# Kernel optimization log

Measured on AMD Instinct MI355X. Metric: run time of the kernel, lower is better.

The kernel has to match this reference:

```python
import jax, jax.numpy as jnp
import numpy as np

N = 50000
IN_DIM = 512
NEG_SLOPE = 0.2


def gat_conv(x, src, dst, W, a_src, a_dst, bias, heads, out_c, concat):
    # x: [N, F_in]; src/dst: [E] (self-loops already appended)
    n = x.shape[0]
    h = (x @ W).reshape(n, heads, out_c)              # [N,H,C]
    alpha_s = (h * a_src).sum(-1)                     # [N,H]
    alpha_d = (h * a_dst).sum(-1)                     # [N,H]
    e = jax.nn.leaky_relu(alpha_s[src] + alpha_d[dst], NEG_SLOPE)  # [E,H]
    # segment softmax over destination node neighborhoods
    m = jax.ops.segment_max(e, dst, num_segments=n)
    e = jnp.exp(e - m[dst])
    denom = jax.ops.segment_sum(e, dst, num_segments=n)
    alpha = e / (denom[dst] + 1e-16)                  # [E,H]
    msg = h[src] * alpha[:, :, None]                  # [E,H,C]
    out = jax.ops.segment_sum(msg, dst, num_segments=n)  # [N,H,C]
    out = out.reshape(n, heads * out_c) if concat else out.mean(axis=1)
    return out + bias


def setup_inputs() -> dict:
    key = jax.random.key(0)
    ks = jax.random.split(key, 16)
    E = 1600000
    txt = jax.random.normal(ks[0], (N, 768), dtype=jnp.float32)
    x = jax.random.normal(ks[1], (N, IN_DIM), dtype=jnp.float32)
    edge_index = jax.random.randint(ks[2], (2, E), 0, N, dtype=jnp.int64)
    s = lambda fan: 1.0 / np.sqrt(fan)
    W1 = jax.random.normal(ks[3], (IN_DIM, 4 * 32), dtype=jnp.float32) * s(IN_DIM)
    a_src1 = jax.random.normal(ks[4], (4, 32), dtype=jnp.float32) * s(32)
    a_dst1 = jax.random.normal(ks[5], (4, 32), dtype=jnp.float32) * s(32)
    b1 = jnp.zeros((4 * 32,), dtype=jnp.float32)
    W2 = jax.random.normal(ks[6], (128, 32), dtype=jnp.float32) * s(128)
    a_src2 = jax.random.normal(ks[7], (1, 32), dtype=jnp.float32) * s(32)
    a_dst2 = jax.random.normal(ks[8], (1, 32), dtype=jnp.float32) * s(32)
    b2 = jnp.zeros((32,), dtype=jnp.float32)
    Wf1 = jax.random.normal(ks[9], (768 + 32, 64), dtype=jnp.float32) * s(800)
    bf1 = jnp.zeros((64,), dtype=jnp.float32)
    Wf2 = jax.random.normal(ks[10], (64, 1), dtype=jnp.float32) * s(64)
    bf2 = jnp.zeros((1,), dtype=jnp.float32)
    return {"txt": txt, "x": x, "W1": W1, "a_src1": a_src1, "a_dst1": a_dst1,
            "b1": b1, "W2": W2, "a_src2": a_src2, "a_dst2": a_dst2, "b2": b2,
            "Wf1": Wf1, "bf1": bf1, "Wf2": Wf2, "bf2": bf2,
            "edge_index": edge_index}


def reference(txt, x, W1, a_src1, a_dst1, b1, W2, a_src2, a_dst2, b2,
              Wf1, bf1, Wf2, bf2, edge_index):
    # PyG GATConv adds self-loops by default
    loops = jnp.arange(N, dtype=edge_index.dtype)
    src = jnp.concatenate([edge_index[0], loops])
    dst = jnp.concatenate([edge_index[1], loops])
    h1 = gat_conv(x, src, dst, W1, a_src1, a_dst1, b1, 4, 32, True)    # [N,128]
    h1 = jax.nn.elu(h1)
    g = gat_conv(h1, src, dst, W2, a_src2, a_dst2, b2, 1, 32, False)   # [N,32]
    z = jnp.concatenate([txt, g], axis=1)                              # [N,800]
    z = jax.nn.relu(z @ Wf1 + bf1)
    out = (z @ Wf2 + bf2).squeeze(-1)                                  # [N]
    return out
```

## Files before the change

### kernel.cpp

```cpp
#include <hip/hip_runtime.h>
#include <hip/hip_bf16.h>
#include <cstdint>

#define NEG_SLOPE 0.2f
#define BCAP 16384

typedef __bf16 bf16_t;
typedef __bf16 bf16x8 __attribute__((ext_vector_type(8)));
typedef float f32x4 __attribute__((ext_vector_type(4)));
typedef float f32x2 __attribute__((ext_vector_type(2)));

__device__ __forceinline__ uint2 pack4bf16(float4 v) {
    ushort u0 = __builtin_bit_cast(ushort, (bf16_t)v.x);
    ushort u1 = __builtin_bit_cast(ushort, (bf16_t)v.y);
    ushort u2 = __builtin_bit_cast(ushort, (bf16_t)v.z);
    ushort u3 = __builtin_bit_cast(ushort, (bf16_t)v.w);
    uint2 r;
    r.x = (uint)u0 | ((uint)u1 << 16);
    r.y = (uint)u2 | ((uint)u3 << 16);
    return r;
}

__device__ __forceinline__ float bflo(uint u) { return __builtin_bit_cast(float, u << 16); }
__device__ __forceinline__ float bfhi(uint u) { return __builtin_bit_cast(float, u & 0xFFFF0000u); }


__device__ void bucket_dev(char* smem, int b, const int* __restrict__ ei, int E, int n,
                           int nbuck, unsigned* __restrict__ gcur, unsigned* __restrict__ gbuck) {
    unsigned* stage = (unsigned*)smem;
    unsigned* cnt   = stage + 4096;
    unsigned* sc    = cnt + 256;
    unsigned* offx  = sc + 256;
    unsigned* gbase = offx + 256;
    int tid = threadIdx.x;
    int ET = E + n;
    int tileStart = b * 4096;
    cnt[tid] = 0;
    __syncthreads();
    unsigned pk[16];
    int rk[16];
    #pragma unroll
    for (int i = 0; i < 16; ++i) {
        int idx = tileStart + i * 256 + tid;
        rk[i] = -1;
        if (idx < ET) {
            int s, d;
            if (idx < E) { s = ei[idx]; d = ei[E + idx]; } else { s = d = idx - E; }
            pk[i] = ((unsigned)d << 16) | (unsigned)s;
            rk[i] = (int)atomicAdd(&cnt[(unsigned)d >> 8], 1u);
        }
    }
    __syncthreads();
    sc[tid] = cnt[tid];
    __syncthreads();
    for (int off = 1; off < 256; off <<= 1) {
        unsigned t = (tid >= off) ? sc[tid - off] : 0u;
        __syncthreads();
        sc[tid] += t;
        __syncthreads();
    }
    offx[tid] = sc[tid] - cnt[tid];
    if (tid < nbuck && cnt[tid] > 0) gbase[tid] = atomicAdd(&gcur[tid], cnt[tid]);
    unsigned total = sc[255];
    __syncthreads();
    #pragma unroll
    for (int i = 0; i < 16; ++i) {
        if (rk[i] >= 0) stage[offx[pk[i] >> 24] + rk[i]] = pk[i];
    }
    __syncthreads();
    for (unsigned j = tid; j < total; j += 256) {
        unsigned p = stage[j];
        unsigned bb = p >> 24;
        unsigned pos = gbase[bb] + (j - offx[bb]);
        gbuck[(size_t)bb * BCAP + pos] = p;
    }
}

__device__ void w1t_dev(char* smem, int b, const float* __restrict__ W, bf16_t* __restrict__ Wt) {
    float (*s)[17] = (float(*)[17])smem;
    int tx = threadIdx.x & 15, ty = threadIdx.x >> 4;
    int kt = b & 31, nt = b >> 5;
    s[ty][tx] = W[(size_t)(kt * 16 + ty) * 128 + nt * 16 + tx];
    __syncthreads();
    Wt[(size_t)(nt * 16 + ty) * 512 + kt * 16 + tx] = (bf16_t)s[tx][ty];
}

__device__ void wf1t_dev(char* smem, int b, const float* __restrict__ W, bf16_t* __restrict__ Wt) {
    float (*s)[17] = (float(*)[17])smem;
    int tx = threadIdx.x & 15, ty = threadIdx.x >> 4;
    int kt = b % 52, nt = b / 52;
    int kg = kt * 16 + ty;
    s[ty][tx] = (kg < 800) ? W[(size_t)kg * 64 + nt * 16 + tx] : 0.f;
    __syncthreads();
    Wt[(size_t)(nt * 16 + ty) * 832 + kt * 16 + tx] = (bf16_t)s[tx][ty];
}

__device__ void finecsr_dev(char* smem, int b, const unsigned* __restrict__ gcur,
                            const unsigned* __restrict__ gbuck, int nbuck,
                            unsigned* __restrict__ rowptr, ushort* __restrict__ csr16) {
    unsigned* s   = (unsigned*)smem;
    unsigned* c   = s + 256;
    unsigned* sc  = c + 256;
    unsigned* cur = sc + 256;
    int tid = threadIdx.x;
    unsigned v = (tid < nbuck) ? gcur[tid] : 0u;
    s[tid] = v;
    __syncthreads();
    for (int off = 1; off < 256; off <<= 1) {
        unsigned t = (tid >= off) ? s[tid - off] : 0u;
        __syncthreads();
        s[tid] += t;
        __syncthreads();
    }
    unsigned base = s[b] - gcur[b];
    unsigned cntL = gcur[b];
    const unsigned* gb = gbuck + (size_t)b * BCAP;
    c[tid] = 0;
    __syncthreads();
    for (unsigned j = tid; j < cntL; j += 256) atomicAdd(&c[(gb[j] >> 16) & 255], 1u);
    __syncthreads();
    sc[tid] = c[tid];
    __syncthreads();
    for (int off = 1; off < 256; off <<= 1) {
        unsigned t = (tid >= off) ? sc[tid - off] : 0u;
        __syncthreads();
        sc[tid] += t;
        __syncthreads();
    }
    unsigned ox = sc[tid] - c[tid];
    rowptr[b * 256 + tid] = base + ox;
    cur[tid] = ox;
    __syncthreads();
    for (unsigned j = tid; j < cntL; j += 256) {
        unsigned p = gb[j];
        unsigned dl = (p >> 16) & 255;
        unsigned pos = atomicAdd(&cur[dl], 1u);
        csr16[base + pos] = (ushort)(p & 0xFFFFu);
    }
}

__device__ void gemm1_dev(char* smem, int b, const float* __restrict__ x,
                          const bf16_t* __restrict__ W1bt,
                          const float* __restrict__ a_src1, const float* __restrict__ a_dst1,
                          unsigned char* __restrict__ h1f8,
                          float* __restrict__ asrc, float* __restrict__ adst, int n) {
    char* As = smem;
    char* Bs = smem + 8192;
    int tid = threadIdx.x;
    int bn = b * 64;
    int wave = tid >> 6, lane = tid & 63;
    int lr = lane & 15, lk = lane >> 4;
    f32x4 acc[8] = {};
    const float4* x4 = (const float4*)x;

    for (int s = 0; s < 8; ++s) {
        int k0 = s * 64;
        #pragma unroll
        for (int i = 0; i < 4; ++i) {
            int v = tid + i * 256;
            int row = v >> 4, c4 = v & 15;
            int node = bn + row;
            float4 val = (node < n) ? x4[(size_t)node * 128 + (k0 >> 2) + c4]
                                    : make_float4(0.f, 0.f, 0.f, 0.f);
            uint off = (uint)(row * 128 + c4 * 8);
            off ^= (uint)((row & 7) << 4);
            *(uint2*)(As + off) = pack4bf16(val);
        }
        #pragma unroll
        for (int i = 0; i < 8; ++i) {
            int v = tid + i * 256;
            int row = v >> 4, c = v & 15;
            uint2 val = *(const uint2*)(W1bt + (size_t)row * 512 + k0 + c * 4);
            uint off = (uint)(row * 128 + c * 8);
            off ^= (uint)((row & 7) << 4);
            *(uint2*)(Bs + off) = val;
        }
        __syncthreads();
        #pragma unroll
        for (int ks = 0; ks < 2; ++ks) {
            uint arow = (uint)(wave * 16 + lr);
            uint aoff = (arow * 128 + (uint)(ks * 64 + lk * 16)) ^ (uint)((lr & 7) << 4);
            bf16x8 av = *(const bf16x8*)(As + aoff);
            #pragma unroll
            for (int f = 0; f < 8; ++f) {
                uint brow = (uint)(f * 16 + lr);
                uint boff = (brow * 128 + (uint)(ks * 64 + lk * 16)) ^ (uint)((lr & 7) << 4);
                bf16x8 bv = *(const bf16x8*)(Bs + boff);
                acc[f] = __builtin_amdgcn_mfma_f32_16x16x32_bf16(av, bv, acc[f], 0, 0, 0);
            }
        }
        __syncthreads();
    }
    #pragma unroll
    for (int f = 0; f < 8; ++f) {
        int nn = f * 16 + lr;
        #pragma unroll
        for (int r = 0; r < 4; ++r) {
            int node = bn + wave * 16 + lk * 4 + r;
            if (node < n) {
                float v = acc[f][r];
                uint b8 = (uint)__builtin_amdgcn_cvt_pk_fp8_f32(v, v, 0, false) & 0xFFu;
                h1f8[(size_t)node * 128 + nn] = (unsigned char)b8;
            }
        }
    }
    float asv[8], adv[8];
    #pragma unroll
    for (int h = 0; h < 4; ++h) {
        asv[2 * h]     = a_src1[h * 32 + lr];
        asv[2 * h + 1] = a_src1[h * 32 + 16 + lr];
        adv[2 * h]     = a_dst1[h * 32 + lr];
        adv[2 * h + 1] = a_dst1[h * 32 + 16 + lr];
    }
    #pragma unroll
    for (int r = 0; r < 4; ++r) {
        int node = bn + wave * 16 + lk * 4 + r;
        #pragma unroll
        for (int h = 0; h < 4; ++h) {
            float ps = acc[2 * h][r] * asv[2 * h] + acc[2 * h + 1][r] * asv[2 * h + 1];
            float pd = acc[2 * h][r] * adv[2 * h] + acc[2 * h + 1][r] * adv[2 * h + 1];
            #pragma unroll
            for (int m = 8; m >= 1; m >>= 1) {
                ps += __shfl_xor(ps, m, 64);
                pd += __shfl_xor(pd, m, 64);
            }
            if (node < n) {
                if (lr == h)     asrc[node * 4 + h] = ps;
                if (lr == h + 4) adst[node * 4 + h] = pd;
            }
        }
    }
}

__device__ void mlpA_dev(char* smem, int b, const float* __restrict__ txt,
                         const bf16_t* __restrict__ Wf1bt, float* __restrict__ hacc, int n) {
    char* As = smem;
    char* Bs = smem + 8192;
    int tid = threadIdx.x;
    int bn = b * 64;
    int wave = tid >> 6, lane = tid & 63;
    int lr = lane & 15, lk = lane >> 4;
    f32x4 acc[4] = {};
    const float4* t4 = (const float4*)txt;
    for (int s = 0; s < 12; ++s) {
        int k0 = s * 64;
        #pragma unroll
        for (int i = 0; i < 4; ++i) {
            int v = tid + i * 256;
            int row = v >> 4, c4 = v & 15;
            int node = bn + row;
            int kg = k0 + c4 * 4;
            float4 val = (node < n) ? t4[(size_t)node * 192 + (kg >> 2)]
                                    : make_float4(0.f, 0.f, 0.f, 0.f);
            uint off = (uint)(row * 128 + c4 * 8);
            off ^= (uint)((row & 7) << 4);
            *(uint2*)(As + off) = pack4bf16(val);
        }
        #pragma unroll
        for (int i = 0; i < 4; ++i) {
            int v = tid + i * 256;
            int row = v >> 4, c = v & 15;
            uint2 val = *(const uint2*)(Wf1bt + (size_t)row * 832 + k0 + c * 4);
            uint off = (uint)(row * 128 + c * 8);
            off ^= (uint)((row & 7) << 4);
            *(uint2*)(Bs + off) = val;
        }
        __syncthreads();
        #pragma unroll
        for (int ks = 0; ks < 2; ++ks) {
            uint arow = (uint)(wave * 16 + lr);
            uint aoff = (arow * 128 + (uint)(ks * 64 + lk * 16)) ^ (uint)((lr & 7) << 4);
            bf16x8 av = *(const bf16x8*)(As + aoff);
            #pragma unroll
            for (int f = 0; f < 4; ++f) {
                uint brow = (uint)(f * 16 + lr);
                uint boff = (brow * 128 + (uint)(ks * 64 + lk * 16)) ^ (uint)((lr & 7) << 4);
                bf16x8 bv = *(const bf16x8*)(Bs + boff);
                acc[f] = __builtin_amdgcn_mfma_f32_16x16x32_bf16(av, bv, acc[f], 0, 0, 0);
            }
        }
        __syncthreads();
    }
    #pragma unroll
    for (int f = 0; f < 4; ++f) {
        int nn = f * 16 + lr;
        #pragma unroll
        for (int r = 0; r < 4; ++r) {
            int node = bn + wave * 16 + lk * 4 + r;
            if (node < n) hacc[(size_t)node * 64 + nn] = acc[f][r];
        }
    }
}

__device__ void gat2_dev(char* smem, int b, const bf16_t* __restrict__ h2bf,
                         const float* __restrict__ asrc2, const float* __restrict__ adst2,
                         const float* __restrict__ b2, const unsigned* __restrict__ rowptr,
                         const ushort* __restrict__ csr16, float* __restrict__ g, int n) {
    ushort* ssm = (ushort*)smem;
    float* psm = (float*)(smem + 512);
    int tid = threadIdx.x;
    int wv = tid >> 6, l = tid & 63;
    int d = b * 4 + wv;
    if (d >= n) return;
    ushort* ss = ssm + wv * 64;
    float* ps = psm + wv * 64;
    unsigned k0 = rowptr[d], k1 = rowptr[d + 1];
    float adh = adst2[d];
    const uint2* h2u2 = (const uint2*)h2bf;
    int c = l & 7, sub = l >> 3;
    float den = 0.f, a0 = 0.f, a1 = 0.f, a2 = 0.f, a3 = 0.f;
    for (unsigned kk = k0; kk < k1; kk += 64) {
        unsigned k = kk + l;
        float p = 0.f;
        unsigned s = 0u;
        if (k < k1) {
            s = csr16[k];
            float v = asrc2[s] + adh;
            v = (v > 0.f) ? v : NEG_SLOPE * v;
            p = __expf(v);
        }
        ss[l] = (ushort)s;
        ps[l] = p;
        den += p;
        int nk = (int)min(64u, k1 - kk);
        for (int qb = 0; qb < nk; qb += 8) {
            int q = qb + sub;
            float pq = ps[q];
            uint2 u = h2u2[(unsigned)ss[q] * 8u + (unsigned)c];
            a0 = fmaf(pq, bflo(u.x), a0);
            a1 = fmaf(pq, bfhi(u.x), a1);
            a2 = fmaf(pq, bflo(u.y), a2);
            a3 = fmaf(pq, bfhi(u.y), a3);
        }
    }
    #pragma unroll
    for (int m = 32; m >= 1; m >>= 1) den += __shfl_xor(den, m, 64);
    #pragma unroll
    for (int m = 8; m <= 32; m <<= 1) {
        a0 += __shfl_xor(a0, m, 64);
        a1 += __shfl_xor(a1, m, 64);
        a2 += __shfl_xor(a2, m, 64);
        a3 += __shfl_xor(a3, m, 64);
    }
    if (l < 8) {
        float inv = 1.f / (den + 1e-16f);
        float4 bb = *(const float4*)(b2 + 4 * c);
        float4 val;
        val.x = a0 * inv + bb.x;
        val.y = a1 * inv + bb.y;
        val.z = a2 * inv + bb.z;
        val.w = a3 * inv + bb.w;
        *(float4*)(g + (size_t)d * 32 + 4 * c) = val;
    }
}


__global__ __launch_bounds__(256) void k_fuse_pre(const int* __restrict__ ei, int E, int n,
                                                  int nbuck, int ntiles,
                                                  unsigned* __restrict__ gcur,
                                                  unsigned* __restrict__ gbuck,
                                                  const float* __restrict__ W1,
                                                  bf16_t* __restrict__ W1bt,
                                                  const float* __restrict__ Wf1,
                                                  bf16_t* __restrict__ Wf1bt) {
    __shared__ __align__(16) char smem[20480];
    int b = blockIdx.x;
    if (b < ntiles)            bucket_dev(smem, b, ei, E, n, nbuck, gcur, gbuck);
    else if (b < ntiles + 256) w1t_dev(smem, b - ntiles, W1, W1bt);
    else                       wf1t_dev(smem, b - ntiles - 256, Wf1, Wf1bt);
}

__global__ __launch_bounds__(256) void k_fuse_csr_gemm(const unsigned* __restrict__ gcur,
                                                       const unsigned* __restrict__ gbuck,
                                                       int nbuck,
                                                       unsigned* __restrict__ rowptr,
                                                       ushort* __restrict__ csr16,
                                                       const float* __restrict__ x,
                                                       const bf16_t* __restrict__ W1bt,
                                                       const float* __restrict__ a_src1,
                                                       const float* __restrict__ a_dst1,
                                                       unsigned char* __restrict__ h1f8,
                                                       float* __restrict__ asrc,
                                                       float* __restrict__ adst, int n) {
    __shared__ __align__(16) char smem[24576];
    int b = blockIdx.x;
    if (b < nbuck) finecsr_dev(smem, b, gcur, gbuck, nbuck, rowptr, csr16);
    else           gemm1_dev(smem, b - nbuck, x, W1bt, a_src1, a_dst1, h1f8, asrc, adst, n);
}

__global__ __launch_bounds__(256) void k_fuse_mlpA_gat2(const float* __restrict__ txt,
                                                        const bf16_t* __restrict__ Wf1bt,
                                                        float* __restrict__ hacc, int nb64,
                                                        const bf16_t* __restrict__ h2bf,
                                                        const float* __restrict__ asrc2,
                                                        const float* __restrict__ adst2,
                                                        const float* __restrict__ b2,
                                                        const unsigned* __restrict__ rowptr,
                                                        const ushort* __restrict__ csr16,
                                                        float* __restrict__ g, int n) {
    __shared__ __align__(16) char smem[16384];
    int b = blockIdx.x;
    if (b < nb64) mlpA_dev(smem, b, txt, Wf1bt, hacc, n);
    else          gat2_dev(smem, b - nb64, h2bf, asrc2, adst2, b2, rowptr, csr16, g, n);
}

__global__ __launch_bounds__(512, 8) void k_gat1(const unsigned char* __restrict__ h1f8,
                                                 const float* __restrict__ asrc,
                                                 const float* __restrict__ adst,
                                                 const float* __restrict__ b1,
                                                 const unsigned* __restrict__ rowptr,
                                                 const ushort* __restrict__ csr16,
                                                 const float* __restrict__ W2,
                                                 const float* __restrict__ a_src2,
                                                 const float* __restrict__ a_dst2,
                                                 bf16_t* __restrict__ h2bf,
                                                 float* __restrict__ asrc2,
                                                 float* __restrict__ adst2, int n) {
    __shared__ float W2l[128 * 32];
    __shared__ ushort ssm[8][64];
    __shared__ float psm[8][64][4];
    int tid = threadIdx.x;
    {
        const float4* w4 = (const float4*)W2;
        float4* wl4 = (float4*)W2l;
        #pragma unroll
        for (int i = 0; i < 2; ++i) wl4[tid + i * 512] = w4[tid + i * 512];
    }
    __syncthreads();
    int wv = tid >> 6, l = tid & 63;
    int d = blockIdx.x * 8 + wv;
    if (d >= n) return;
    ushort* ss = ssm[wv];
    unsigned k0 = rowptr[d], k1 = rowptr[d + 1];
    float4 ad4 = *(const float4*)(adst + (size_t)d * 4);
    const float4* asrc4 = (const float4*)asrc;
    const uint2* h1u2 = (const uint2*)h1f8;
    int c16 = l & 15, sub = l >> 4;
    int hd = c16 >> 2;
    float den0 = 0.f, den1 = 0.f, den2 = 0.f, den3 = 0.f;
    float a[8] = {};
    for (unsigned kk = k0; kk < k1; kk += 64) {
        unsigned k = kk + l;
        float p0 = 0.f, p1 = 0.f, p2 = 0.f, p3 = 0.f;
        unsigned s = 0u;
        if (k < k1) {
            s = csr16[k];
            float4 av = asrc4[s];
            float v0 = av.x + ad4.x; v0 = (v0 > 0.f) ? v0 : NEG_SLOPE * v0; p0 = __expf(v0);
            float v1 = av.y + ad4.y; v1 = (v1 > 0.f) ? v1 : NEG_SLOPE * v1; p1 = __expf(v1);
            float v2 = av.z + ad4.z; v2 = (v2 > 0.f) ? v2 : NEG_SLOPE * v2; p2 = __expf(v2);
            float v3 = av.w + ad4.w; v3 = (v3 > 0.f) ? v3 : NEG_SLOPE * v3; p3 = __expf(v3);
        }
        ss[l] = (ushort)s;
        float4 pv; pv.x = p0; pv.y = p1; pv.z = p2; pv.w = p3;
        *(float4*)psm[wv][l] = pv;
        den0 += p0; den1 += p1; den2 += p2; den3 += p3;
        int nk = (int)min(64u, k1 - kk);
        for (int qb = 0; qb < nk; qb += 4) {
            int q = qb + sub;
            float pq = psm[wv][q][hd];
            unsigned sq = ss[q];
            uint2 u = h1u2[sq * 16u + (unsigned)c16];
            f32x2 v0 = __builtin_amdgcn_cvt_pk_f32_fp8(u.x, false);
            f32x2 v1 = __builtin_amdgcn_cvt_pk_f32_fp8(u.x, true);
            f32x2 v2 = __builtin_amdgcn_cvt_pk_f32_fp8(u.y, false);
            f32x2 v3 = __builtin_amdgcn_cvt_pk_f32_fp8(u.y, true);
            a[0] = fmaf(pq, v0.x, a[0]); a[1] = fmaf(pq, v0.y, a[1]);
            a[2] = fmaf(pq, v1.x, a[2]); a[3] = fmaf(pq, v1.y, a[3]);
            a[4] = fmaf(pq, v2.x, a[4]); a[5] = fmaf(pq, v2.y, a[5]);
            a[6] = fmaf(pq, v3.x, a[6]); a[7] = fmaf(pq, v3.y, a[7]);
        }
    }
    #pragma unroll
    for (int m = 32; m >= 1; m >>= 1) {
        den0 += __shfl_xor(den0, m, 64);
        den1 += __shfl_xor(den1, m, 64);
        den2 += __shfl_xor(den2, m, 64);
        den3 += __shfl_xor(den3, m, 64);
    }
    #pragma unroll
    for (int i = 0; i < 8; ++i) {
        a[i] += __shfl_xor(a[i], 16, 64);
        a[i] += __shfl_xor(a[i], 32, 64);
    }
    float denh = (hd == 0) ? den0 : (hd == 1) ? den1 : (hd == 2) ? den2 : den3;
    float inv = 1.f / (denh + 1e-16f);
    float* os = (float*)psm[wv];
    if (sub == 0) {
        float4 ba = *(const float4*)(b1 + 8 * c16);
        float4 bbv = *(const float4*)(b1 + 8 * c16 + 4);
        float o0 = a[0] * inv + ba.x;  o0 = (o0 > 0.f) ? o0 : (__expf(o0) - 1.f);
        float o1 = a[1] * inv + ba.y;  o1 = (o1 > 0.f) ? o1 : (__expf(o1) - 1.f);
        float o2 = a[2] * inv + ba.z;  o2 = (o2 > 0.f) ? o2 : (__expf(o2) - 1.f);
        float o3 = a[3] * inv + ba.w;  o3 = (o3 > 0.f) ? o3 : (__expf(o3) - 1.f);
        float o4 = a[4] * inv + bbv.x; o4 = (o4 > 0.f) ? o4 : (__expf(o4) - 1.f);
        float o5 = a[5] * inv + bbv.y; o5 = (o5 > 0.f) ? o5 : (__expf(o5) - 1.f);
        float o6 = a[6] * inv + bbv.z; o6 = (o6 > 0.f) ? o6 : (__expf(o6) - 1.f);
        float o7 = a[7] * inv + bbv.w; o7 = (o7 > 0.f) ? o7 : (__expf(o7) - 1.f);
        float4 ov0; ov0.x = o0; ov0.y = o1; ov0.z = o2; ov0.w = o3;
        float4 ov1; ov1.x = o4; ov1.y = o5; ov1.z = o6; ov1.w = o7;
        *(float4*)(os + 8 * c16) = ov0;
        *(float4*)(os + 8 * c16 + 4) = ov1;
    }
    int j32 = l & 31, kh = l >> 5;
    float part = 0.f;
    const float4* os4 = (const float4*)(os + kh * 64);
    #pragma unroll 4
    for (int i = 0; i < 16; ++i) {
        float4 ov = os4[i];
        int kb = kh * 64 + i * 4;
        part += ov.x * W2l[(kb + 0) * 32 + j32] + ov.y * W2l[(kb + 1) * 32 + j32]
              + ov.z * W2l[(kb + 2) * 32 + j32] + ov.w * W2l[(kb + 3) * 32 + j32];
    }
    part += __shfl_xor(part, 32, 64);
    float h2v = part;
    float cs = h2v * a_src2[j32];
    float cd = h2v * a_dst2[j32];
    #pragma unroll
    for (int m = 16; m >= 1; m >>= 1) {
        cs += __shfl_xor(cs, m, 64);
        cd += __shfl_xor(cd, m, 64);
    }
    if (l < 32) h2bf[(size_t)d * 32 + l] = (bf16_t)h2v;
    if (l == 0) { asrc2[d] = cs; adst2[d] = cd; }
}

__global__ __launch_bounds__(256) void k_mlpB(const float* __restrict__ g,
                                              const bf16_t* __restrict__ Wf1bt,
                                              const float* __restrict__ hacc,
                                              const float* __restrict__ bf1,
                                              const float* __restrict__ Wf2,
                                              const float* __restrict__ bf2,
                                              float* __restrict__ out, int n) {
    __shared__ __align__(16) char smem[16384];
    char* As = smem;
    char* Bs = smem + 8192;
    int tid = threadIdx.x;
    int bn = blockIdx.x * 64;
    int wave = tid >> 6, lane = tid & 63;
    int lr = lane & 15, lk = lane >> 4;
    const float4* g4 = (const float4*)g;
    #pragma unroll
    for (int i = 0; i < 4; ++i) {
        int v = tid + i * 256;
        int row = v >> 4, c4 = v & 15;
        int node = bn + row;
        int kg = 768 + c4 * 4;
        float4 val = make_float4(0.f, 0.f, 0.f, 0.f);
        if (node < n && kg < 800) val = g4[(size_t)node * 8 + ((kg - 768) >> 2)];
        uint off = (uint)(row * 128 + c4 * 8);
        off ^= (uint)((row & 7) << 4);
        *(uint2*)(As + off) = pack4bf16(val);
    }
    #pragma unroll
    for (int i = 0; i < 4; ++i) {
        int v = tid + i * 256;
        int row = v >> 4, c = v & 15;
        uint2 val = *(const uint2*)(Wf1bt + (size_t)row * 832 + 768 + c * 4);
        uint off = (uint)(row * 128 + c * 8);
        off ^= (uint)((row & 7) << 4);
        *(uint2*)(Bs + off) = val;
    }
    f32x4 acc[4];
    #pragma unroll
    for (int f = 0; f < 4; ++f) {
        int nn = f * 16 + lr;
        #pragma unroll
        for (int r = 0; r < 4; ++r) {
            int node = bn + wave * 16 + lk * 4 + r;
            acc[f][r] = (node < n) ? hacc[(size_t)node * 64 + nn] : 0.f;
        }
    }
    __syncthreads();
    #pragma unroll
    for (int ks = 0; ks < 2; ++ks) {
        uint arow = (uint)(wave * 16 + lr);
        uint aoff = (arow * 128 + (uint)(ks * 64 + lk * 16)) ^ (uint)((lr & 7) << 4);
        bf16x8 av = *(const bf16x8*)(As + aoff);
        #pragma unroll
        for (int f = 0; f < 4; ++f) {
            uint brow = (uint)(f * 16 + lr);
            uint boff = (brow * 128 + (uint)(ks * 64 + lk * 16)) ^ (uint)((lr & 7) << 4);
            bf16x8 bv = *(const bf16x8*)(Bs + boff);
            acc[f] = __builtin_amdgcn_mfma_f32_16x16x32_bf16(av, bv, acc[f], 0, 0, 0);
        }
    }
    float rsum[4] = {0.f, 0.f, 0.f, 0.f};
    #pragma unroll
    for (int f = 0; f < 4; ++f) {
        int nn = f * 16 + lr;
        float bb = bf1[nn], ww = Wf2[nn];
        #pragma unroll
        for (int r = 0; r < 4; ++r) {
            float v = acc[f][r] + bb;
            rsum[r] += fmaxf(v, 0.f) * ww;
        }
    }
    #pragma unroll
    for (int r = 0; r < 4; ++r) {
        #pragma unroll
        for (int m = 8; m >= 1; m >>= 1) rsum[r] += __shfl_xor(rsum[r], m, 64);
        if (lr == 0) {
            int node = bn + wave * 16 + lk * 4 + r;
            if (node < n) out[node] = rsum[r] + bf2[0];
        }
    }
}

extern "C" void kernel_launch(void* const* d_in, const int* in_sizes, int n_in,
                              void* d_out, int out_size, void* d_ws, size_t ws_size,
                              hipStream_t stream) {
    const float* txt    = (const float*)d_in[0];
    const float* x      = (const float*)d_in[1];
    const float* W1     = (const float*)d_in[2];
    const float* a_src1 = (const float*)d_in[3];
    const float* a_dst1 = (const float*)d_in[4];
    const float* b1     = (const float*)d_in[5];
    const float* W2     = (const float*)d_in[6];
    const float* a_src2 = (const float*)d_in[7];
    const float* a_dst2 = (const float*)d_in[8];
    const float* b2     = (const float*)d_in[9];
    const float* Wf1    = (const float*)d_in[10];
    const float* bf1    = (const float*)d_in[11];
    const float* Wf2    = (const float*)d_in[12];
    const float* bf2    = (const float*)d_in[13];
    const int*   ei     = (const int*)d_in[14];

    int n  = in_sizes[1] / 512;
    int E  = in_sizes[14] / 2;
    int ET = E + n;
    int nbuck = (n + 255) >> 8;
    float* out = (float*)d_out;

    char* p = (char*)d_ws;
    auto alloc = [&](size_t bytes) -> char* {
        char* q = p;
        p += (bytes + 255) & ~(size_t)255;
        return q;
    };
    unsigned char* h1f8 = (unsigned char*)alloc((size_t)n * 128);
    float*    asrc1  = (float*)alloc((size_t)n * 4 * 4);
    float*    adst1  = (float*)alloc((size_t)n * 4 * 4);
    bf16_t*   h2bf   = (bf16_t*)alloc((size_t)n * 32 * 2);
    float*    asrc2  = (float*)alloc((size_t)n * 4);
    float*    adst2  = (float*)alloc((size_t)n * 4);
    float*    gbuf   = (float*)alloc((size_t)n * 32 * 4);
    float*    hacc   = (float*)alloc((size_t)n * 64 * 4);
    unsigned* rowptr = (unsigned*)alloc((size_t)(nbuck * 256 + 1) * 4);
    ushort*   csr16  = (ushort*)alloc((size_t)ET * 2);
    unsigned* gbuck  = (unsigned*)alloc((size_t)nbuck * BCAP * 4);
    unsigned* gcur   = (unsigned*)alloc((size_t)nbuck * 4);
    bf16_t*   W1bt   = (bf16_t*)alloc((size_t)128 * 512 * 2);
    bf16_t*   Wf1bt  = (bf16_t*)alloc((size_t)64 * 832 * 2);

    hipMemsetAsync(gcur, 0, (size_t)nbuck * 4, stream);

    int ntiles = (ET + 4095) / 4096;
    int nb64 = (n + 63) / 64;
    int nb8 = (n + 7) / 8;
    int nb4 = (n + 3) / 4;

    k_fuse_pre<<<ntiles + 256 + 208, 256, 0, stream>>>(ei, E, n, nbuck, ntiles,
                                                       gcur, gbuck, W1, W1bt, Wf1, Wf1bt);
    k_fuse_csr_gemm<<<nbuck + nb64, 256, 0, stream>>>(gcur, gbuck, nbuck, rowptr, csr16,
                                                      x, W1bt, a_src1, a_dst1, h1f8,
                                                      asrc1, adst1, n);
    k_gat1<<<nb8, 512, 0, stream>>>(h1f8, asrc1, adst1, b1, rowptr, csr16,
                                    W2, a_src2, a_dst2, h2bf, asrc2, adst2, n);
    k_fuse_mlpA_gat2<<<nb64 + nb4, 256, 0, stream>>>(txt, Wf1bt, hacc, nb64,
                                                     h2bf, asrc2, adst2, b2,
                                                     rowptr, csr16, gbuf, n);
    k_mlpB<<<nb64, 256, 0, stream>>>(gbuf, Wf1bt, hacc, bf1, Wf2, bf2, out, n);
}
```

Baseline: 205.1 us.

## Co-schedule text MLP GEMM with GAT layer-1 instead of GAT layer-2

Moves the independent txt@Wf1 GEMM (mlpA) out of the launch it shared with GAT layer-2 and into the GAT layer-1 launch. Both sides now run as 512-thread blocks, with mlpA reworked to handle 128-row tiles. GAT layer-2 becomes its own small kernel. The aim is to overlap the compute-bound GEMM with the longer, latency-bound layer-1 gather, at the cost of larger shared memory per block in the fused kernel and a standalone gat2 launch.

```diff
diff --git a/kernel.cpp b/kernel.cpp
--- a/kernel.cpp
+++ b/kernel.cpp
@@ -232,12 +232,129 @@
     }
 }
 
-__device__ void mlpA_dev(char* smem, int b, const float* __restrict__ txt,
-                         const bf16_t* __restrict__ Wf1bt, float* __restrict__ hacc, int n) {
+__device__ void gat1_dev(char* smem, int b, const unsigned char* __restrict__ h1f8,
+                         const float* __restrict__ asrc, const float* __restrict__ adst,
+                         const float* __restrict__ b1, const unsigned* __restrict__ rowptr,
+                         const ushort* __restrict__ csr16, const float* __restrict__ W2,
+                         const float* __restrict__ a_src2, const float* __restrict__ a_dst2,
+                         bf16_t* __restrict__ h2bf, float* __restrict__ asrc2,
+                         float* __restrict__ adst2, int n) {
+    float* psmf = (float*)smem;
+    float* W2l = (float*)(smem + 8192);
+    ushort* ssm = (ushort*)(smem + 24576);
+    int tid = threadIdx.x;
+    {
+        const float4* w4 = (const float4*)W2;
+        float4* wl4 = (float4*)W2l;
+        #pragma unroll
+        for (int i = 0; i < 2; ++i) wl4[tid + i * 512] = w4[tid + i * 512];
+    }
+    __syncthreads();
+    int wv = tid >> 6, l = tid & 63;
+    int d = b * 8 + wv;
+    if (d >= n) return;
+    ushort* ss = ssm + wv * 64;
+    float* psw = psmf + wv * 256;
+    unsigned k0 = rowptr[d], k1 = rowptr[d + 1];
+    float4 ad4 = *(const float4*)(adst + (size_t)d * 4);
+    const float4* asrc4 = (const float4*)asrc;
+    const uint2* h1u2 = (const uint2*)h1f8;
+    int c16 = l & 15, sub = l >> 4;
+    int hd = c16 >> 2;
+    float den0 = 0.f, den1 = 0.f, den2 = 0.f, den3 = 0.f;
+    float a[8] = {};
+    for (unsigned kk = k0; kk < k1; kk += 64) {
+        unsigned k = kk + l;
+        float p0 = 0.f, p1 = 0.f, p2 = 0.f, p3 = 0.f;
+        unsigned s = 0u;
+        if (k < k1) {
+            s = csr16[k];
+            float4 av = asrc4[s];
+            float v0 = av.x + ad4.x; v0 = (v0 > 0.f) ? v0 : NEG_SLOPE * v0; p0 = __expf(v0);
+            float v1 = av.y + ad4.y; v1 = (v1 > 0.f) ? v1 : NEG_SLOPE * v1; p1 = __expf(v1);
+            float v2 = av.z + ad4.z; v2 = (v2 > 0.f) ? v2 : NEG_SLOPE * v2; p2 = __expf(v2);
+            float v3 = av.w + ad4.w; v3 = (v3 > 0.f) ? v3 : NEG_SLOPE * v3; p3 = __expf(v3);
+        }
+        ss[l] = (ushort)s;
+        float4 pv; pv.x = p0; pv.y = p1; pv.z = p2; pv.w = p3;
+        *(float4*)(psw + l * 4) = pv;
+        den0 += p0; den1 += p1; den2 += p2; den3 += p3;
+        int nk = (int)min(64u, k1 - kk);
+        for (int qb = 0; qb < nk; qb += 4) {
+            int q = qb + sub;
+            float pq = psw[q * 4 + hd];
+            unsigned sq = ss[q];
+            uint2 u = h1u2[sq * 16u + (unsigned)c16];
+            f32x2 v0 = __builtin_amdgcn_cvt_pk_f32_fp8(u.x, false);
+            f32x2 v1 = __builtin_amdgcn_cvt_pk_f32_fp8(u.x, true);
+            f32x2 v2 = __builtin_amdgcn_cvt_pk_f32_fp8(u.y, false);
+            f32x2 v3 = __builtin_amdgcn_cvt_pk_f32_fp8(u.y, true);
+            a[0] = fmaf(pq, v0.x, a[0]); a[1] = fmaf(pq, v0.y, a[1]);
+            a[2] = fmaf(pq, v1.x, a[2]); a[3] = fmaf(pq, v1.y, a[3]);
+            a[4] = fmaf(pq, v2.x, a[4]); a[5] = fmaf(pq, v2.y, a[5]);
+            a[6] = fmaf(pq, v3.x, a[6]); a[7] = fmaf(pq, v3.y, a[7]);
+        }
+    }
+    #pragma unroll
+    for (int m = 32; m >= 1; m >>= 1) {
+        den0 += __shfl_xor(den0, m, 64);
+        den1 += __shfl_xor(den1, m, 64);
+        den2 += __shfl_xor(den2, m, 64);
+        den3 += __shfl_xor(den3, m, 64);
+    }
+    #pragma unroll
+    for (int i = 0; i < 8; ++i) {
+        a[i] += __shfl_xor(a[i], 16, 64);
+        a[i] += __shfl_xor(a[i], 32, 64);
+    }
+    float denh = (hd == 0) ? den0 : (hd == 1) ? den1 : (hd == 2) ? den2 : den3;
+    float inv = 1.f / (denh + 1e-16f);
+    float* os = psw;
+    if (sub == 0) {
+        float4 ba = *(const float4*)(b1 + 8 * c16);
+        float4 bbv = *(const float4*)(b1 + 8 * c16 + 4);
+        float o0 = a[0] * inv + ba.x;  o0 = (o0 > 0.f) ? o0 : (__expf(o0) - 1.f);
+        float o1 = a[1] * inv + ba.y;  o1 = (o1 > 0.f) ? o1 : (__expf(o1) - 1.f);
+        float o2 = a[2] * inv + ba.z;  o2 = (o2 > 0.f) ? o2 : (__expf(o2) - 1.f);
+        float o3 = a[3] * inv + ba.w;  o3 = (o3 > 0.f) ? o3 : (__expf(o3) - 1.f);
+        float o4 = a[4] * inv + bbv.x; o4 = (o4 > 0.f) ? o4 : (__expf(o4) - 1.f);
+        float o5 = a[5] * inv + bbv.y; o5 = (o5 > 0.f) ? o5 : (__expf(o5) - 1.f);
+        float o6 = a[6] * inv + bbv.z; o6 = (o6 > 0.f) ? o6 : (__expf(o6) - 1.f);
+        float o7 = a[7] * inv + bbv.w; o7 = (o7 > 0.f) ? o7 : (__expf(o7) - 1.f);
+        float4 ov0; ov0.x = o0; ov0.y = o1; ov0.z = o2; ov0.w = o3;
+        float4 ov1; ov1.x = o4; ov1.y = o5; ov1.z = o6; ov1.w = o7;
+        *(float4*)(os + 8 * c16) = ov0;
+        *(float4*)(os + 8 * c16 + 4) = ov1;
+    }
+    int j32 = l & 31, kh = l >> 5;
+    float part = 0.f;
+    const float4* os4 = (const float4*)(os + kh * 64);
+    #pragma unroll 4
+    for (int i = 0; i < 16; ++i) {
+        float4 ov = os4[i];
+        int kb = kh * 64 + i * 4;
+        part += ov.x * W2l[(kb + 0) * 32 + j32] + ov.y * W2l[(kb + 1) * 32 + j32]
+              + ov.z * W2l[(kb + 2) * 32 + j32] + ov.w * W2l[(kb + 3) * 32 + j32];
+    }
+    part += __shfl_xor(part, 32, 64);
+    float h2v = part;
+    float cs = h2v * a_src2[j32];
+    float cd = h2v * a_dst2[j32];
+    #pragma unroll
+    for (int m = 16; m >= 1; m >>= 1) {
+        cs += __shfl_xor(cs, m, 64);
+        cd += __shfl_xor(cd, m, 64);
+    }
+    if (l < 32) h2bf[(size_t)d * 32 + l] = (bf16_t)h2v;
+    if (l == 0) { asrc2[d] = cs; adst2[d] = cd; }
+}
+
+__device__ void mlpA2_dev(char* smem, int b, const float* __restrict__ txt,
+                          const bf16_t* __restrict__ Wf1bt, float* __restrict__ hacc, int n) {
     char* As = smem;
-    char* Bs = smem + 8192;
+    char* Bs = smem + 16384;
     int tid = threadIdx.x;
-    int bn = b * 64;
+    int bn = b * 128;
     int wave = tid >> 6, lane = tid & 63;
     int lr = lane & 15, lk = lane >> 4;
     f32x4 acc[4] = {};
@@ -246,7 +363,7 @@
         int k0 = s * 64;
         #pragma unroll
         for (int i = 0; i < 4; ++i) {
-            int v = tid + i * 256;
+            int v = tid + i * 512;
             int row = v >> 4, c4 = v & 15;
             int node = bn + row;
             int kg = k0 + c4 * 4;
@@ -257,8 +374,8 @@
             *(uint2*)(As + off) = pack4bf16(val);
         }
         #pragma unroll
-        for (int i = 0; i < 4; ++i) {
-            int v = tid + i * 256;
+        for (int i = 0; i < 2; ++i) {
+            int v = tid + i * 512;
             int row = v >> 4, c = v & 15;
             uint2 val = *(const uint2*)(Wf1bt + (size_t)row * 832 + k0 + c * 4);
             uint off = (uint)(row * 128 + c * 8);
@@ -388,141 +505,32 @@
     else           gemm1_dev(smem, b - nbuck, x, W1bt, a_src1, a_dst1, h1f8, asrc, adst, n);
 }
 
-__global__ __launch_bounds__(256) void k_fuse_mlpA_gat2(const float* __restrict__ txt,
-                                                        const bf16_t* __restrict__ Wf1bt,
-                                                        float* __restrict__ hacc, int nb64,
-                                                        const bf16_t* __restrict__ h2bf,
-                                                        const float* __restrict__ asrc2,
-                                                        const float* __restrict__ adst2,
-                                                        const float* __restrict__ b2,
-                                                        const unsigned* __restrict__ rowptr,
-                                                        const ushort* __restrict__ csr16,
-                                                        float* __restrict__ g, int n) {
-    __shared__ __align__(16) char smem[16384];
+__global__ __launch_bounds__(512, 8) void k_fuse_gat1_mlpA(
+        const unsigned char* __restrict__ h1f8,
+        const float* __restrict__ asrc, const float* __restrict__ adst,
+        const float* __restrict__ b1, const unsigned* __restrict__ rowptr,
+        const ushort* __restrict__ csr16, const float* __restrict__ W2,
+        const float* __restrict__ a_src2, const float* __restrict__ a_dst2,
+        bf16_t* __restrict__ h2bf, float* __restrict__ asrc2,
+        float* __restrict__ adst2, int nb8,
+        const float* __restrict__ txt, const bf16_t* __restrict__ Wf1bt,
+        float* __restrict__ hacc, int n) {
+    __shared__ __align__(16) char smem[25600];
     int b = blockIdx.x;
-    if (b < nb64) mlpA_dev(smem, b, txt, Wf1bt, hacc, n);
-    else          gat2_dev(smem, b - nb64, h2bf, asrc2, adst2, b2, rowptr, csr16, g, n);
-}
-
-__global__ __launch_bounds__(512, 8) void k_gat1(const unsigned char* __restrict__ h1f8,
-                                                 const float* __restrict__ asrc,
-                                                 const float* __restrict__ adst,
-                                                 const float* __restrict__ b1,
+    if (b < nb8) gat1_dev(smem, b, h1f8, asrc, adst, b1, rowptr, csr16,
+                          W2, a_src2, a_dst2, h2bf, asrc2, adst2, n);
+    else         mlpA2_dev(smem, b - nb8, txt, Wf1bt, hacc, n);
+}
+
+__global__ __launch_bounds__(256, 8) void k_gat2(const bf16_t* __restrict__ h2bf,
+                                                 const float* __restrict__ asrc2,
+                                                 const float* __restrict__ adst2,
+                                                 const float* __restrict__ b2,
                                                  const unsigned* __restrict__ rowptr,
                                                  const ushort* __restrict__ csr16,
-                                                 const float* __restrict__ W2,
-                                                 const float* __restrict__ a_src2,
-                                                 const float* __restrict__ a_dst2,
-                                                 bf16_t* __restrict__ h2bf,
-                                                 float* __restrict__ asrc2,
-                                                 float* __restrict__ adst2, int n) {
-    __shared__ float W2l[128 * 32];
-    __shared__ ushort ssm[8][64];
-    __shared__ float psm[8][64][4];
-    int tid = threadIdx.x;
-    {
-        const float4* w4 = (const float4*)W2;
-        float4* wl4 = (float4*)W2l;
-        #pragma unroll
-        for (int i = 0; i < 2; ++i) wl4[tid + i * 512] = w4[tid + i * 512];
-    }
-    __syncthreads();
-    int wv = tid >> 6, l = tid & 63;
-    int d = blockIdx.x * 8 + wv;
-    if (d >= n) return;
-    ushort* ss = ssm[wv];
-    unsigned k0 = rowptr[d], k1 = rowptr[d + 1];
-    float4 ad4 = *(const float4*)(adst + (size_t)d * 4);
-    const float4* asrc4 = (const float4*)asrc;
-    const uint2* h1u2 = (const uint2*)h1f8;
-    int c16 = l & 15, sub = l >> 4;
-    int hd = c16 >> 2;
-    float den0 = 0.f, den1 = 0.f, den2 = 0.f, den3 = 0.f;
-    float a[8] = {};
-    for (unsigned kk = k0; kk < k1; kk += 64) {
-        unsigned k = kk + l;
-        float p0 = 0.f, p1 = 0.f, p2 = 0.f, p3 = 0.f;
-        unsigned s = 0u;
-        if (k < k1) {
-            s = csr16[k];
-            float4 av = asrc4[s];
-            float v0 = av.x + ad4.x; v0 = (v0 > 0.f) ? v0 : NEG_SLOPE * v0; p0 = __expf(v0);
-            float v1 = av.y + ad4.y; v1 = (v1 > 0.f) ? v1 : NEG_SLOPE * v1; p1 = __expf(v1);
-            float v2 = av.z + ad4.z; v2 = (v2 > 0.f) ? v2 : NEG_SLOPE * v2; p2 = __expf(v2);
-            float v3 = av.w + ad4.w; v3 = (v3 > 0.f) ? v3 : NEG_SLOPE * v3; p3 = __expf(v3);
-        }
-        ss[l] = (ushort)s;
-        float4 pv; pv.x = p0; pv.y = p1; pv.z = p2; pv.w = p3;
-        *(float4*)psm[wv][l] = pv;
-        den0 += p0; den1 += p1; den2 += p2; den3 += p3;
-        int nk = (int)min(64u, k1 - kk);
-        for (int qb = 0; qb < nk; qb += 4) {
-            int q = qb + sub;
-            float pq = psm[wv][q][hd];
-            unsigned sq = ss[q];
-            uint2 u = h1u2[sq * 16u + (unsigned)c16];
-            f32x2 v0 = __builtin_amdgcn_cvt_pk_f32_fp8(u.x, false);
-            f32x2 v1 = __builtin_amdgcn_cvt_pk_f32_fp8(u.x, true);
-            f32x2 v2 = __builtin_amdgcn_cvt_pk_f32_fp8(u.y, false);
-            f32x2 v3 = __builtin_amdgcn_cvt_pk_f32_fp8(u.y, true);
-            a[0] = fmaf(pq, v0.x, a[0]); a[1] = fmaf(pq, v0.y, a[1]);
-            a[2] = fmaf(pq, v1.x, a[2]); a[3] = fmaf(pq, v1.y, a[3]);
-            a[4] = fmaf(pq, v2.x, a[4]); a[5] = fmaf(pq, v2.y, a[5]);
-            a[6] = fmaf(pq, v3.x, a[6]); a[7] = fmaf(pq, v3.y, a[7]);
-        }
-    }
-    #pragma unroll
-    for (int m = 32; m >= 1; m >>= 1) {
-        den0 += __shfl_xor(den0, m, 64);
-        den1 += __shfl_xor(den1, m, 64);
-        den2 += __shfl_xor(den2, m, 64);
-        den3 += __shfl_xor(den3, m, 64);
-    }
-    #pragma unroll
-    for (int i = 0; i < 8; ++i) {
-        a[i] += __shfl_xor(a[i], 16, 64);
-        a[i] += __shfl_xor(a[i], 32, 64);
-    }
-    float denh = (hd == 0) ? den0 : (hd == 1) ? den1 : (hd == 2) ? den2 : den3;
-    float inv = 1.f / (denh + 1e-16f);
-    float* os = (float*)psm[wv];
-    if (sub == 0) {
-        float4 ba = *(const float4*)(b1 + 8 * c16);
-        float4 bbv = *(const float4*)(b1 + 8 * c16 + 4);
-        float o0 = a[0] * inv + ba.x;  o0 = (o0 > 0.f) ? o0 : (__expf(o0) - 1.f);
-        float o1 = a[1] * inv + ba.y;  o1 = (o1 > 0.f) ? o1 : (__expf(o1) - 1.f);
-        float o2 = a[2] * inv + ba.z;  o2 = (o2 > 0.f) ? o2 : (__expf(o2) - 1.f);
-        float o3 = a[3] * inv + ba.w;  o3 = (o3 > 0.f) ? o3 : (__expf(o3) - 1.f);
-        float o4 = a[4] * inv + bbv.x; o4 = (o4 > 0.f) ? o4 : (__expf(o4) - 1.f);
-        float o5 = a[5] * inv + bbv.y; o5 = (o5 > 0.f) ? o5 : (__expf(o5) - 1.f);
-        float o6 = a[6] * inv + bbv.z; o6 = (o6 > 0.f) ? o6 : (__expf(o6) - 1.f);
-        float o7 = a[7] * inv + bbv.w; o7 = (o7 > 0.f) ? o7 : (__expf(o7) - 1.f);
-        float4 ov0; ov0.x = o0; ov0.y = o1; ov0.z = o2; ov0.w = o3;
-        float4 ov1; ov1.x = o4; ov1.y = o5; ov1.z = o6; ov1.w = o7;
-        *(float4*)(os + 8 * c16) = ov0;
-        *(float4*)(os + 8 * c16 + 4) = ov1;
-    }
-    int j32 = l & 31, kh = l >> 5;
-    float part = 0.f;
-    const float4* os4 = (const float4*)(os + kh * 64);
-    #pragma unroll 4
-    for (int i = 0; i < 16; ++i) {
-        float4 ov = os4[i];
-        int kb = kh * 64 + i * 4;
-        part += ov.x * W2l[(kb + 0) * 32 + j32] + ov.y * W2l[(kb + 1) * 32 + j32]
-              + ov.z * W2l[(kb + 2) * 32 + j32] + ov.w * W2l[(kb + 3) * 32 + j32];
-    }
-    part += __shfl_xor(part, 32, 64);
-    float h2v = part;
-    float cs = h2v * a_src2[j32];
-    float cd = h2v * a_dst2[j32];
-    #pragma unroll
-    for (int m = 16; m >= 1; m >>= 1) {
-        cs += __shfl_xor(cs, m, 64);
-        cd += __shfl_xor(cd, m, 64);
-    }
-    if (l < 32) h2bf[(size_t)d * 32 + l] = (bf16_t)h2v;
-    if (l == 0) { asrc2[d] = cs; adst2[d] = cd; }
+                                                 float* __restrict__ g, int n) {
+    __shared__ __align__(16) char smem[1536];
+    gat2_dev(smem, blockIdx.x, h2bf, asrc2, adst2, b2, rowptr, csr16, g, n);
 }
 
 __global__ __launch_bounds__(256) void k_mlpB(const float* __restrict__ g,
@@ -659,16 +667,16 @@
     int nb64 = (n + 63) / 64;
     int nb8 = (n + 7) / 8;
     int nb4 = (n + 3) / 4;
+    int nb128 = (n + 127) / 128;
 
     k_fuse_pre<<<ntiles + 256 + 208, 256, 0, stream>>>(ei, E, n, nbuck, ntiles,
                                                        gcur, gbuck, W1, W1bt, Wf1, Wf1bt);
     k_fuse_csr_gemm<<<nbuck + nb64, 256, 0, stream>>>(gcur, gbuck, nbuck, rowptr, csr16,
                                                       x, W1bt, a_src1, a_dst1, h1f8,
                                                       asrc1, adst1, n);
-    k_gat1<<<nb8, 512, 0, stream>>>(h1f8, asrc1, adst1, b1, rowptr, csr16,
-                                    W2, a_src2, a_dst2, h2bf, asrc2, adst2, n);
-    k_fuse_mlpA_gat2<<<nb64 + nb4, 256, 0, stream>>>(txt, Wf1bt, hacc, nb64,
-                                                     h2bf, asrc2, adst2, b2,
-                                                     rowptr, csr16, gbuf, n);
+    k_fuse_gat1_mlpA<<<nb8 + nb128, 512, 0, stream>>>(h1f8, asrc1, adst1, b1, rowptr, csr16,
+                                                      W2, a_src2, a_dst2, h2bf, asrc2, adst2,
+                                                      nb8, txt, Wf1bt, hacc, n);
+    k_gat2<<<nb4, 256, 0, stream>>>(h2bf, asrc2, adst2, b2, rowptr, csr16, gbuf, n);
     k_mlpB<<<nb64, 256, 0, stream>>>(gbuf, Wf1bt, hacc, bf1, Wf2, bf2, out, n);
 }
```

New measurement: 215.1 us. 4.9% more time.

## Move mlpA into CSR/GEMM1 launch and split gat2 into its own kernel

Applied to the files above, without the earlier changes.

The txt@Wf1 partial GEMM (mlpA) now runs as extra blocks in the CSR-build/GEMM1 fused launch instead of alongside gat2, so it overlaps with earlier independent work. gat2 becomes a standalone kernel with small static shared memory and launch bounds allowing higher occupancy, rather than sharing a 16KB-smem heterogeneous kernel. The risk is a heavier first fused kernel and different block scheduling balance between the two launches.

```diff
diff --git a/kernel.cpp b/kernel.cpp
--- a/kernel.cpp
+++ b/kernel.cpp
@@ -292,68 +292,6 @@
     }
 }
 
-__device__ void gat2_dev(char* smem, int b, const bf16_t* __restrict__ h2bf,
-                         const float* __restrict__ asrc2, const float* __restrict__ adst2,
-                         const float* __restrict__ b2, const unsigned* __restrict__ rowptr,
-                         const ushort* __restrict__ csr16, float* __restrict__ g, int n) {
-    ushort* ssm = (ushort*)smem;
-    float* psm = (float*)(smem + 512);
-    int tid = threadIdx.x;
-    int wv = tid >> 6, l = tid & 63;
-    int d = b * 4 + wv;
-    if (d >= n) return;
-    ushort* ss = ssm + wv * 64;
-    float* ps = psm + wv * 64;
-    unsigned k0 = rowptr[d], k1 = rowptr[d + 1];
-    float adh = adst2[d];
-    const uint2* h2u2 = (const uint2*)h2bf;
-    int c = l & 7, sub = l >> 3;
-    float den = 0.f, a0 = 0.f, a1 = 0.f, a2 = 0.f, a3 = 0.f;
-    for (unsigned kk = k0; kk < k1; kk += 64) {
-        unsigned k = kk + l;
-        float p = 0.f;
-        unsigned s = 0u;
-        if (k < k1) {
-            s = csr16[k];
-            float v = asrc2[s] + adh;
-            v = (v > 0.f) ? v : NEG_SLOPE * v;
-            p = __expf(v);
-        }
-        ss[l] = (ushort)s;
-        ps[l] = p;
-        den += p;
-        int nk = (int)min(64u, k1 - kk);
-        for (int qb = 0; qb < nk; qb += 8) {
-            int q = qb + sub;
-            float pq = ps[q];
-            uint2 u = h2u2[(unsigned)ss[q] * 8u + (unsigned)c];
-            a0 = fmaf(pq, bflo(u.x), a0);
-            a1 = fmaf(pq, bfhi(u.x), a1);
-            a2 = fmaf(pq, bflo(u.y), a2);
-            a3 = fmaf(pq, bfhi(u.y), a3);
-        }
-    }
-    #pragma unroll
-    for (int m = 32; m >= 1; m >>= 1) den += __shfl_xor(den, m, 64);
-    #pragma unroll
-    for (int m = 8; m <= 32; m <<= 1) {
-        a0 += __shfl_xor(a0, m, 64);
-        a1 += __shfl_xor(a1, m, 64);
-        a2 += __shfl_xor(a2, m, 64);
-        a3 += __shfl_xor(a3, m, 64);
-    }
-    if (l < 8) {
-        float inv = 1.f / (den + 1e-16f);
-        float4 bb = *(const float4*)(b2 + 4 * c);
-        float4 val;
-        val.x = a0 * inv + bb.x;
-        val.y = a1 * inv + bb.y;
-        val.z = a2 * inv + bb.z;
-        val.w = a3 * inv + bb.w;
-        *(float4*)(g + (size_t)d * 32 + 4 * c) = val;
-    }
-}
-
 
 __global__ __launch_bounds__(256) void k_fuse_pre(const int* __restrict__ ei, int E, int n,
                                                   int nbuck, int ntiles,
@@ -370,38 +308,21 @@
     else                       wf1t_dev(smem, b - ntiles - 256, Wf1, Wf1bt);
 }
 
-__global__ __launch_bounds__(256) void k_fuse_csr_gemm(const unsigned* __restrict__ gcur,
-                                                       const unsigned* __restrict__ gbuck,
-                                                       int nbuck,
-                                                       unsigned* __restrict__ rowptr,
-                                                       ushort* __restrict__ csr16,
-                                                       const float* __restrict__ x,
-                                                       const bf16_t* __restrict__ W1bt,
-                                                       const float* __restrict__ a_src1,
-                                                       const float* __restrict__ a_dst1,
-                                                       unsigned char* __restrict__ h1f8,
-                                                       float* __restrict__ asrc,
-                                                       float* __restrict__ adst, int n) {
+__global__ __launch_bounds__(256) void k_fuse_csr_gemm_mlpA(
+        const unsigned* __restrict__ gcur, const unsigned* __restrict__ gbuck, int nbuck,
+        unsigned* __restrict__ rowptr, ushort* __restrict__ csr16,
+        const float* __restrict__ x, const bf16_t* __restrict__ W1bt,
+        const float* __restrict__ a_src1, const float* __restrict__ a_dst1,
+        unsigned char* __restrict__ h1f8, float* __restrict__ asrc,
+        float* __restrict__ adst, int nb64,
+        const float* __restrict__ txt, const bf16_t* __restrict__ Wf1bt,
+        float* __restrict__ hacc, int n) {
     __shared__ __align__(16) char smem[24576];
     int b = blockIdx.x;
-    if (b < nbuck) finecsr_dev(smem, b, gcur, gbuck, nbuck, rowptr, csr16);
-    else           gemm1_dev(smem, b - nbuck, x, W1bt, a_src1, a_dst1, h1f8, asrc, adst, n);
-}
-
-__global__ __launch_bounds__(256) void k_fuse_mlpA_gat2(const float* __restrict__ txt,
-                                                        const bf16_t* __restrict__ Wf1bt,
-                                                        float* __restrict__ hacc, int nb64,
-                                                        const bf16_t* __restrict__ h2bf,
-                                                        const float* __restrict__ asrc2,
-                                                        const float* __restrict__ adst2,
-                                                        const float* __restrict__ b2,
-                                                        const unsigned* __restrict__ rowptr,
-                                                        const ushort* __restrict__ csr16,
-                                                        float* __restrict__ g, int n) {
-    __shared__ __align__(16) char smem[16384];
-    int b = blockIdx.x;
-    if (b < nb64) mlpA_dev(smem, b, txt, Wf1bt, hacc, n);
-    else          gat2_dev(smem, b - nb64, h2bf, asrc2, adst2, b2, rowptr, csr16, g, n);
+    if (b < nbuck)              finecsr_dev(smem, b, gcur, gbuck, nbuck, rowptr, csr16);
+    else if (b < nbuck + nb64)  gemm1_dev(smem, b - nbuck, x, W1bt, a_src1, a_dst1,
+                                          h1f8, asrc, adst, n);
+    else                        mlpA_dev(smem, b - nbuck - nb64, txt, Wf1bt, hacc, n);
 }
 
 __global__ __launch_bounds__(512, 8) void k_gat1(const unsigned char* __restrict__ h1f8,
@@ -525,6 +446,71 @@
     if (l == 0) { asrc2[d] = cs; adst2[d] = cd; }
 }
 
+__global__ __launch_bounds__(256, 8) void k_gat2(const bf16_t* __restrict__ h2bf,
+                                                 const float* __restrict__ asrc2,
+                                                 const float* __restrict__ adst2,
+                                                 const float* __restrict__ b2,
+                                                 const unsigned* __restrict__ rowptr,
+                                                 const ushort* __restrict__ csr16,
+                                                 float* __restrict__ g, int n) {
+    __shared__ ushort ssm[4][64];
+    __shared__ float psm[4][64];
+    int tid = threadIdx.x;
+    int wv = tid >> 6, l = tid & 63;
+    int d = blockIdx.x * 4 + wv;
+    if (d >= n) return;
+    ushort* ss = ssm[wv];
+    float* ps = psm[wv];
+    unsigned k0 = rowptr[d], k1 = rowptr[d + 1];
+    float adh = adst2[d];
+    const uint2* h2u2 = (const uint2*)h2bf;
+    int c = l & 7, sub = l >> 3;
+    float den = 0.f, a0 = 0.f, a1 = 0.f, a2 = 0.f, a3 = 0.f;
+    for (unsigned kk = k0; kk < k1; kk += 64) {
+        unsigned k = kk + l;
+        float p = 0.f;
+        unsigned s = 0u;
+        if (k < k1) {
+            s = csr16[k];
+            float v = asrc2[s] + adh;
+            v = (v > 0.f) ? v : NEG_SLOPE * v;
+            p = __expf(v);
+        }
+        ss[l] = (ushort)s;
+        ps[l] = p;
+        den += p;
+        int nk = (int)min(64u, k1 - kk);
+        for (int qb = 0; qb < nk; qb += 8) {
+            int q = qb + sub;
+            float pq = ps[q];
+            uint2 u = h2u2[(unsigned)ss[q] * 8u + (unsigned)c];
+            a0 = fmaf(pq, bflo(u.x), a0);
+            a1 = fmaf(pq, bfhi(u.x), a1);
+            a2 = fmaf(pq, bflo(u.y), a2);
+            a3 = fmaf(pq, bfhi(u.y), a3);
+        }
+    }
+    #pragma unroll
+    for (int m = 32; m >= 1; m >>= 1) den += __shfl_xor(den, m, 64);
+    #pragma unroll
+    for (int m = 8; m <= 32; m <<= 1) {
+        a0 += __shfl_xor(a0, m, 64);
+        a1 += __shfl_xor(a1, m, 64);
+        a2 += __shfl_xor(a2, m, 64);
+        a3 += __shfl_xor(a3, m, 64);
+    }
+    if (l < 8) {
+        float inv = 1.f / (den + 1e-16f);
+        float4 bb = *(const float4*)(b2 + 4 * c);
+        float4 val;
+        val.x = a0 * inv + bb.x;
+        val.y = a1 * inv + bb.y;
+        val.z = a2 * inv + bb.z;
+        val.w = a3 * inv + bb.w;
+        *(float4*)(g + (size_t)d * 32 + 4 * c) = val;
+    }
+}
+
 __global__ __launch_bounds__(256) void k_mlpB(const float* __restrict__ g,
                                               const bf16_t* __restrict__ Wf1bt,
                                               const float* __restrict__ hacc,
@@ -662,13 +648,12 @@
 
     k_fuse_pre<<<ntiles + 256 + 208, 256, 0, stream>>>(ei, E, n, nbuck, ntiles,
                                                        gcur, gbuck, W1, W1bt, Wf1, Wf1bt);
-    k_fuse_csr_gemm<<<nbuck + nb64, 256, 0, stream>>>(gcur, gbuck, nbuck, rowptr, csr16,
-                                                      x, W1bt, a_src1, a_dst1, h1f8,
-                                                      asrc1, adst1, n);
+    k_fuse_csr_gemm_mlpA<<<nbuck + nb64 + nb64, 256, 0, stream>>>(
+        gcur, gbuck, nbuck, rowptr, csr16,
+        x, W1bt, a_src1, a_dst1, h1f8, asrc1, adst1, nb64,
+        txt, Wf1bt, hacc, n);
     k_gat1<<<nb8, 512, 0, stream>>>(h1f8, asrc1, adst1, b1, rowptr, csr16,
                                     W2, a_src2, a_dst2, h2bf, asrc2, adst2, n);
-    k_fuse_mlpA_gat2<<<nb64 + nb4, 256, 0, stream>>>(txt, Wf1bt, hacc, nb64,
-                                                     h2bf, asrc2, adst2, b2,
-                                                     rowptr, csr16, gbuf, n);
+    k_gat2<<<nb4, 256, 0, stream>>>(h2bf, asrc2, adst2, b2, rowptr, csr16, gbuf, n);
     k_mlpB<<<nb64, 256, 0, stream>>>(gbuf, Wf1bt, hacc, bf1, Wf2, bf2, out, n);
 }
```

Result: slower. 213.0 us (+3.8%).
